# Performance work log

Measured on AMD Instinct MI355X. Metric: run time of the kernel, lower is better.

Reference implementation:

```python
import jax, jax.numpy as jnp
import numpy as np

N_NODES = 100_000
N_EDGES = 1_600_000
D_IN = 128
D_HID = 64   # hard-coded hidden width in Embedder.__init__
D_OUT = 128  # embed_dim
N_GRAPHS = 512


def setup_inputs() -> dict:
    key = jax.random.key(0)
    ks = jax.random.split(key, 10)
    x = jax.random.normal(ks[0], (N_NODES, D_IN), dtype=jnp.float32)
    edge_index = jax.random.randint(ks[1], (2, N_EDGES), 0, N_NODES, dtype=jnp.int64)
    batch_index = jnp.sort(jax.random.randint(ks[2], (N_NODES,), 0, N_GRAPHS, dtype=jnp.int64))
    def glorot(k, fan_in, fan_out):
        s = 1.0 / np.sqrt(fan_in)
        return jax.random.uniform(k, (fan_in, fan_out), jnp.float32, -s, s)
    # layer 1: SAGEConv(D_IN -> D_HID); layer 2: SAGEConv(D_HID -> D_OUT)
    return {
        "x": x,
        "W1_l": glorot(ks[3], D_IN, D_HID),   # applied to mean-aggregated neighbors
        "W1_r": glorot(ks[4], D_IN, D_HID),   # applied to root node
        "b1": jnp.zeros((D_HID,), jnp.float32),
        "W2_l": glorot(ks[5], D_HID, D_OUT),
        "W2_r": glorot(ks[6], D_HID, D_OUT),
        "b2": jnp.zeros((D_OUT,), jnp.float32),
        "edge_index": edge_index,
        "batch_index": batch_index,
    }


def _sage_conv(x, edge_index, W_l, W_r, b):
    # PyG SAGEConv with mean aggregation:
    # out_i = (mean_{j in N(i)} x_j) @ W_l + x_i @ W_r + b
    src, dst = edge_index[0], edge_index[1]
    n = x.shape[0]
    agg = jax.ops.segment_sum(x[src], dst, num_segments=n)          # [N, F]
    deg = jax.ops.segment_sum(jnp.ones((src.shape[0],), x.dtype), dst, num_segments=n)
    mean_nbr = agg / jnp.maximum(deg, 1.0)[:, None]
    return mean_nbr @ W_l + x @ W_r + b


def reference(x, W1_l, W1_r, b1, W2_l, W2_r, b2, edge_index, batch_index):
    h = _sage_conv(x, edge_index, W1_l, W1_r, b1)
    h = jax.nn.relu(h)
    h = _sage_conv(h, edge_index, W2_l, W2_r, b2)
    # F.dropout(p=0.5, training=False) -> identity in eval mode
    # gap: global mean pool per graph
    sums = jax.ops.segment_sum(h, batch_index, num_segments=N_GRAPHS)
    cnts = jax.ops.segment_sum(jnp.ones((h.shape[0],), h.dtype), batch_index, num_segments=N_GRAPHS)
    return sums / jnp.maximum(cnts, 1.0)[:, None]
```

## Files before the change

kernel.cpp:

```cpp
#include <hip/hip_runtime.h>

#define NN   100000
#define NE   1600000
#define DIN  128
#define DH   64
#define DOUT 128
#define NG   512

#define NB   391
#define EPB  6250
#define MSZ  (NB*256)

typedef short short8 __attribute__((ext_vector_type(8)));
typedef float floatx4 __attribute__((ext_vector_type(4)));

__device__ __forceinline__ unsigned short f2bf(float f) {
  unsigned b = __float_as_uint(f);
  b += 0x7FFF + ((b >> 16) & 1);
  return (unsigned short)(b >> 16);
}
__device__ __forceinline__ float bflo(unsigned u) {
  return __uint_as_float(u << 16);
}
__device__ __forceinline__ float bfhi(unsigned u) {
  return __uint_as_float(u & 0xFFFF0000u);
}
__device__ __forceinline__ unsigned pack2(float a, float b) {
  return (unsigned)f2bf(a) | ((unsigned)f2bf(b) << 16);
}

__global__ __launch_bounds__(256) void prep_kernel(
    const int* __restrict__ dst, int* __restrict__ cnt,
    const float* __restrict__ W1l, const float* __restrict__ W1r,
    short* __restrict__ wfrag, const int* __restrict__ batch,
    int* __restrict__ gs) {
  __shared__ int h[NB];
  int b = blockIdx.x;
  if (b < 256) {
    for (int i = threadIdx.x; i < NB; i += 256) h[i] = 0;
    __syncthreads();
    int start = b * EPB, end = start + EPB;
    for (int e = start + threadIdx.x; e < end; e += 256)
      atomicAdd(&h[dst[e] >> 8], 1);
    __syncthreads();
    for (int bb = threadIdx.x; bb < NB; bb += 256)
      cnt[bb * 256 + b] = h[bb];
  } else if (b == 256) {
    for (int i = threadIdx.x; i < DIN * DH; i += 256) {
      int k = i >> 6, n = i & 63;
      int kt = k >> 5, kin = k & 31;
      int lane = ((kin >> 3) << 4) | (n & 15);
      int j8 = kin & 7;
      int jt = n >> 4;
      float wl = W1l[i], wr = W1r[i];
      unsigned bl_ = __float_as_uint(wl);
      unsigned br_ = __float_as_uint(wr);
      short hl = (short)(bl_ >> 16);
      short hr = (short)(br_ >> 16);
      float rl = wl - __uint_as_float(bl_ & 0xFFFF0000u);
      float rr = wr - __uint_as_float(br_ & 0xFFFF0000u);
      short ll = (short)(__float_as_uint(rl) >> 16);
      short lr = (short)(__float_as_uint(rr) >> 16);
      int base0 = (((kt * 2 + 0) * 4 + jt) * 2) * 512 + lane * 8 + j8;
      int base1 = (((kt * 2 + 1) * 4 + jt) * 2) * 512 + lane * 8 + j8;
      wfrag[base0]       = hl;
      wfrag[base0 + 512] = ll;
      wfrag[base1]       = hr;
      wfrag[base1 + 512] = lr;
    }
  } else {
    for (int g = threadIdx.x; g <= NG; g += 256) {
      if (g == NG) { gs[NG] = NN; continue; }
      int lo = 0, hi = NN;
      while (lo < hi) {
        int mid = (lo + hi) >> 1;
        if (batch[mid] < g) lo = mid + 1; else hi = mid;
      }
      gs[g] = lo;
    }
  }
}

__global__ __launch_bounds__(256) void reduce_kernel(
    const int* __restrict__ cnt, int* __restrict__ partials) {
  __shared__ int s[256];
  int i = blockIdx.x * 256 + threadIdx.x;
  s[threadIdx.x] = cnt[i];
  __syncthreads();
  for (int off = 128; off > 0; off >>= 1) {
    if (threadIdx.x < off) s[threadIdx.x] += s[threadIdx.x + off];
    __syncthreads();
  }
  if (threadIdx.x == 0) partials[blockIdx.x] = s[0];
}

__global__ __launch_bounds__(256) void scanpart_kernel(int* __restrict__ partials) {
  __shared__ int s[NB];
  for (int i = threadIdx.x; i < NB; i += 256) s[i] = partials[i];
  __syncthreads();
  if (threadIdx.x == 0) {
    int run = 0;
    for (int i = 0; i < NB; ++i) { int v = s[i]; s[i] = run; run += v; }
  }
  __syncthreads();
  for (int i = threadIdx.x; i < NB; i += 256) partials[i] = s[i];
}

__global__ __launch_bounds__(256) void scanfinal_kernel(
    const int* __restrict__ cnt, const int* __restrict__ partials,
    int* __restrict__ scanned) {
  __shared__ int s[256];
  int t = threadIdx.x;
  int i = blockIdx.x * 256 + t;
  int c = cnt[i];
  s[t] = c;
  __syncthreads();
  for (int off = 1; off < 256; off <<= 1) {
    int v = (t >= off) ? s[t - off] : 0;
    __syncthreads();
    s[t] += v;
    __syncthreads();
  }
  scanned[i] = s[t] - c + partials[blockIdx.x];
}

__global__ __launch_bounds__(1024) void part_kernel(
    const int* __restrict__ src, const int* __restrict__ dst,
    const int* __restrict__ scanned, int* __restrict__ part) {
  __shared__ int cur[NB];
  int b = blockIdx.x;
  for (int i = threadIdx.x; i < NB; i += 1024)
    cur[i] = scanned[i * 256 + b];
  __syncthreads();
  int start = b * EPB, end = start + EPB;
  for (int e = start + threadIdx.x; e < end; e += 1024) {
    int d = dst[e], s = src[e];
    int pos = atomicAdd(&cur[d >> 8], 1);
    part[pos] = ((d & 255) << 17) | s;
  }
}

__global__ __launch_bounds__(256, 5) void proj_kernel(
    const float* __restrict__ x, const short* __restrict__ wfrag,
    const float* __restrict__ b1, unsigned short* __restrict__ xlb,
    unsigned short* __restrict__ xrb) {
  __shared__ short sB[16384];
  int wave = threadIdx.x >> 6;
  int lane = threadIdx.x & 63;
  int m = lane & 15, q = lane >> 4;
  int tile = blockIdx.x * 4 + wave;
  bool act = tile < 6250;
  int tc = act ? tile : 6249;

  int r0 = tc * 16 + m;
  const float4* xa = (const float4*)x + (size_t)r0 * 32 + q * 2;

  floatx4 acc[8];
#pragma unroll
  for (int a = 0; a < 8; ++a) acc[a] = (floatx4){0.f, 0.f, 0.f, 0.f};

  const float4* wf4 = (const float4*)wfrag;
  float4* sB4 = (float4*)sB;

#pragma unroll 1
  for (int stage = 0; stage < 2; ++stage) {
    if (stage) __syncthreads();
    for (int i = threadIdx.x; i < 2048; i += 256)
      sB4[i] = wf4[stage * 2048 + i];
    __syncthreads();

#pragma unroll
    for (int kk = 0; kk < 2; ++kk) {
      int kt = stage * 2 + kk;
      float4 p0 = xa[kt * 8];
      float4 p1 = xa[kt * 8 + 1];
      float af0[8] = {p0.x, p0.y, p0.z, p0.w, p1.x, p1.y, p1.z, p1.w};
      short8 ah, al;
#pragma unroll
      for (int e = 0; e < 8; ++e) {
        unsigned b0 = __float_as_uint(af0[e]);
        ah[e] = (short)(b0 >> 16);
        float lo0 = af0[e] - __uint_as_float(b0 & 0xFFFF0000u);
        al[e] = (short)(__float_as_uint(lo0) >> 16);
      }
#pragma unroll
      for (int mat = 0; mat < 2; ++mat) {
#pragma unroll
        for (int jt = 0; jt < 4; ++jt) {
          int unit = ((kk * 2 + mat) * 4 + jt) * 2;
          short8 bh = *(const short8*)(sB + unit * 512 + lane * 8);
          short8 bl = *(const short8*)(sB + (unit + 1) * 512 + lane * 8);
          floatx4 c = acc[mat * 4 + jt];
          c = __builtin_amdgcn_mfma_f32_16x16x32_bf16(ah, bh, c, 0, 0, 0);
          c = __builtin_amdgcn_mfma_f32_16x16x32_bf16(ah, bl, c, 0, 0, 0);
          c = __builtin_amdgcn_mfma_f32_16x16x32_bf16(al, bh, c, 0, 0, 0);
          acc[mat * 4 + jt] = c;
        }
      }
    }
  }

  if (act) {
#pragma unroll
    for (int jt = 0; jt < 4; ++jt) {
      int j = jt * 16 + m;
      float bj = b1[j];
      floatx4 cl = acc[jt], cr = acc[4 + jt];
#pragma unroll
      for (int r = 0; r < 4; ++r) {
        int n0 = tile * 16 + q * 4 + r;
        xlb[(size_t)n0 * DH + j] = f2bf(cl[r]);
        xrb[(size_t)n0 * DH + j] = f2bf(cr[r] + bj);
      }
    }
  }
}

__global__ __launch_bounds__(256) void bucket_csr_kernel(
    const int* __restrict__ part, const int* __restrict__ scanned,
    int* __restrict__ row_start, int* __restrict__ eidx) {
  int b = blockIdx.x, t = threadIdx.x;
  int ebeg = scanned[b * 256];
  int eend = (b == NB - 1) ? NE : scanned[(b + 1) * 256];
  int nbase = b << 8;
  int nloc = NN - nbase; if (nloc > 256) nloc = 256;
  __shared__ int cntL[256];
  __shared__ int exclL[256];
  cntL[t] = 0;
  __syncthreads();
  for (int e = ebeg + t; e < eend; e += 256)
    atomicAdd(&cntL[part[e] >> 17], 1);
  __syncthreads();
  int c = cntL[t];
  exclL[t] = c;
  __syncthreads();
  for (int off = 1; off < 256; off <<= 1) {
    int v = (t >= off) ? exclL[t - off] : 0;
    __syncthreads();
    exclL[t] += v;
    __syncthreads();
  }
  int excl = exclL[t] - c;
  if (t < nloc) row_start[nbase + t] = ebeg + excl;
  if (b == NB - 1 && t == 0) row_start[NN] = NE;
  cntL[t] = excl;
  __syncthreads();
  for (int e = ebeg + t; e < eend; e += 256) {
    int v = part[e];
    int pos = atomicAdd(&cntL[v >> 17], 1);
    eidx[ebeg + pos] = v & 0x1FFFF;
  }
}

template <bool RELU_ADD>
__global__ __launch_bounds__(256) void gather_kernel(
    const uint4* __restrict__ feat4, const int* __restrict__ row_start,
    const int* __restrict__ eidx, const uint4* __restrict__ xr4,
    uint4* __restrict__ out4) {
  int t = blockIdx.x * 256 + threadIdx.x;
  int node = t >> 3;
  if (node >= NN) return;
  int fl = t & 7;
  int rs = row_start[node], re = row_start[node + 1];
  float a0 = 0.f, a1 = 0.f, a2 = 0.f, a3 = 0.f;
  float a4 = 0.f, a5 = 0.f, a6 = 0.f, a7 = 0.f;
  int k = rs;
  for (; k + 8 <= re; k += 8) {
    uint4 v[8];
#pragma unroll
    for (int u = 0; u < 8; ++u) v[u] = feat4[(size_t)eidx[k + u] * 8 + fl];
#pragma unroll
    for (int u = 0; u < 8; ++u) {
      a0 += bflo(v[u].x); a1 += bfhi(v[u].x);
      a2 += bflo(v[u].y); a3 += bfhi(v[u].y);
      a4 += bflo(v[u].z); a5 += bfhi(v[u].z);
      a6 += bflo(v[u].w); a7 += bfhi(v[u].w);
    }
  }
  for (; k + 2 <= re; k += 2) {
    uint4 v0 = feat4[(size_t)eidx[k] * 8 + fl];
    uint4 v1 = feat4[(size_t)eidx[k + 1] * 8 + fl];
    a0 += bflo(v0.x) + bflo(v1.x); a1 += bfhi(v0.x) + bfhi(v1.x);
    a2 += bflo(v0.y) + bflo(v1.y); a3 += bfhi(v0.y) + bfhi(v1.y);
    a4 += bflo(v0.z) + bflo(v1.z); a5 += bfhi(v0.z) + bfhi(v1.z);
    a6 += bflo(v0.w) + bflo(v1.w); a7 += bfhi(v0.w) + bfhi(v1.w);
  }
  if (k < re) {
    uint4 v = feat4[(size_t)eidx[k] * 8 + fl];
    a0 += bflo(v.x); a1 += bfhi(v.x);
    a2 += bflo(v.y); a3 += bfhi(v.y);
    a4 += bflo(v.z); a5 += bfhi(v.z);
    a6 += bflo(v.w); a7 += bfhi(v.w);
  }
  float inv = 1.0f / fmaxf((float)(re - rs), 1.0f);
  a0 *= inv; a1 *= inv; a2 *= inv; a3 *= inv;
  a4 *= inv; a5 *= inv; a6 *= inv; a7 *= inv;
  if (RELU_ADD) {
    uint4 r = xr4[(size_t)node * 8 + fl];
    a0 = fmaxf(a0 + bflo(r.x), 0.f); a1 = fmaxf(a1 + bfhi(r.x), 0.f);
    a2 = fmaxf(a2 + bflo(r.y), 0.f); a3 = fmaxf(a3 + bfhi(r.y), 0.f);
    a4 = fmaxf(a4 + bflo(r.z), 0.f); a5 = fmaxf(a5 + bfhi(r.z), 0.f);
    a6 = fmaxf(a6 + bflo(r.w), 0.f); a7 = fmaxf(a7 + bfhi(r.w), 0.f);
  }
  uint4 o;
  o.x = pack2(a0, a1);
  o.y = pack2(a2, a3);
  o.z = pack2(a4, a5);
  o.w = pack2(a6, a7);
  out4[(size_t)node * 8 + fl] = o;
}

__global__ __launch_bounds__(256) void pool_final_kernel(
    const unsigned* __restrict__ hb2, const unsigned* __restrict__ mb2,
    const int* __restrict__ gs, const float* __restrict__ W2l,
    const float* __restrict__ W2r, const float* __restrict__ b2,
    float* __restrict__ out) {
  int g = blockIdx.x;
  int start = gs[g], end = gs[g + 1];
  int slot = threadIdx.x >> 5;
  int j2   = threadIdx.x & 31;
  float sh0 = 0.f, sh1 = 0.f, sm0 = 0.f, sm1 = 0.f;
  for (int n = start + slot; n < end; n += 8) {
    unsigned hv = hb2[(size_t)n * 32 + j2];
    unsigned mv = mb2[(size_t)n * 32 + j2];
    sh0 += bflo(hv); sh1 += bfhi(hv);
    sm0 += bflo(mv); sm1 += bfhi(mv);
  }
  __shared__ float redh[8][DH];
  __shared__ float redm[8][DH];
  redh[slot][j2 * 2] = sh0; redh[slot][j2 * 2 + 1] = sh1;
  redm[slot][j2 * 2] = sm0; redm[slot][j2 * 2 + 1] = sm1;
  __syncthreads();
  __shared__ float hsL[DH], msL[DH];
  if (threadIdx.x < DH) {
    float a = 0.f, b = 0.f;
#pragma unroll
    for (int s = 0; s < 8; ++s) { a += redh[s][threadIdx.x]; b += redm[s][threadIdx.x]; }
    hsL[threadIdx.x] = a; msL[threadIdx.x] = b;
  }
  __syncthreads();
  int j = threadIdx.x;
  if (j < DOUT) {
    float n = (float)(end - start);
    float acc = 0.f;
#pragma unroll 8
    for (int k = 0; k < DH; ++k)
      acc += msL[k] * W2l[k * DOUT + j] + hsL[k] * W2r[k * DOUT + j];
    out[g * DOUT + j] = (acc + n * b2[j]) / fmaxf(n, 1.0f);
  }
}

extern "C" void kernel_launch(void* const* d_in, const int* in_sizes, int n_in,
                              void* d_out, int out_size, void* d_ws, size_t ws_size,
                              hipStream_t stream) {
  (void)in_sizes; (void)n_in; (void)out_size; (void)ws_size;
  const float* x   = (const float*)d_in[0];
  const float* W1l = (const float*)d_in[1];
  const float* W1r = (const float*)d_in[2];
  const float* b1  = (const float*)d_in[3];
  const float* W2l = (const float*)d_in[4];
  const float* W2r = (const float*)d_in[5];
  const float* b2  = (const float*)d_in[6];
  const int*   ei  = (const int*)d_in[7];
  const int*   batch = (const int*)d_in[8];
  const int* src = ei;
  const int* dst = ei + NE;
  float* out = (float*)d_out;

  char* ws = (char*)d_ws;
  unsigned short* xlb = (unsigned short*)(ws);
  unsigned short* hb  = (unsigned short*)(ws + 12800000);
  unsigned short* mb  = (unsigned short*)(ws + 25600000);
  unsigned short* xrb = (unsigned short*)(ws + 38400000);
  int*  part      = (int*)(ws + 51200000);
  int*  cnt       = (int*)(ws + 57600000);
  int*  scanned   = (int*)(ws + 58000384);
  int*  eidx      = (int*)(ws + 76800000);
  int*  row_start = (int*)(ws + 83200000);
  int*   gs       = (int*)(ws + 83600128);
  short* wfrag    = (short*)(ws + 83900032);
  int*  partials  = (int*)(ws + 84400128);

  const int gBlocks = (NN * 8 + 255) / 256;

  prep_kernel<<<258, 256, 0, stream>>>(dst, cnt, W1l, W1r, wfrag, batch, gs);
  reduce_kernel<<<NB, 256, 0, stream>>>(cnt, partials);
  scanpart_kernel<<<1, 256, 0, stream>>>(partials);
  scanfinal_kernel<<<NB, 256, 0, stream>>>(cnt, partials, scanned);

  proj_kernel<<<1563, 256, 0, stream>>>(x, wfrag, b1, xlb, xrb);
  part_kernel<<<256, 1024, 0, stream>>>(src, dst, scanned, part);
  bucket_csr_kernel<<<NB, 256, 0, stream>>>(part, scanned, row_start, eidx);

  gather_kernel<true><<<gBlocks, 256, 0, stream>>>(
      (const uint4*)xlb, row_start, eidx, (const uint4*)xrb, (uint4*)hb);

  gather_kernel<false><<<gBlocks, 256, 0, stream>>>(
      (const uint4*)hb, row_start, eidx, nullptr, (uint4*)mb);

  pool_final_kernel<<<NG, 256, 0, stream>>>(
      (const unsigned*)hb, (const unsigned*)mb, gs, W2l, W2r, b2, out);
}
```

Measured before the change: 252.1 us.

## Build CSR with global per-node atomics and fuse scatter into projection kernel

After: 430.4 us. +70.7%, slower.

```diff
diff --git a/kernel.cpp b/kernel.cpp
--- a/kernel.cpp
+++ b/kernel.cpp
@@ -8,8 +8,8 @@
 #define NG   512
 
 #define NB   391
-#define EPB  6250
 #define MSZ  (NB*256)
+#define SCB  1024
 
 typedef short short8 __attribute__((ext_vector_type(8)));
 typedef float floatx4 __attribute__((ext_vector_type(4)));
@@ -30,22 +30,14 @@
 }
 
 __global__ __launch_bounds__(256) void prep_kernel(
-    const int* __restrict__ dst, int* __restrict__ cnt,
+    int* __restrict__ deg,
     const float* __restrict__ W1l, const float* __restrict__ W1r,
     short* __restrict__ wfrag, const int* __restrict__ batch,
     int* __restrict__ gs) {
-  __shared__ int h[NB];
   int b = blockIdx.x;
-  if (b < 256) {
-    for (int i = threadIdx.x; i < NB; i += 256) h[i] = 0;
-    __syncthreads();
-    int start = b * EPB, end = start + EPB;
-    for (int e = start + threadIdx.x; e < end; e += 256)
-      atomicAdd(&h[dst[e] >> 8], 1);
-    __syncthreads();
-    for (int bb = threadIdx.x; bb < NB; bb += 256)
-      cnt[bb * 256 + b] = h[bb];
-  } else if (b == 256) {
+  if (b < NB) {
+    deg[b * 256 + threadIdx.x] = 0;
+  } else if (b == NB) {
     for (int i = threadIdx.x; i < DIN * DH; i += 256) {
       int k = i >> 6, n = i & 63;
       int kt = k >> 5, kin = k & 31;
@@ -81,11 +73,18 @@
   }
 }
 
+__global__ __launch_bounds__(1024) void hist_kernel(
+    const int* __restrict__ dst, int* __restrict__ deg) {
+  int stride = gridDim.x * 1024;
+  for (int e = blockIdx.x * 1024 + threadIdx.x; e < NE; e += stride)
+    atomicAdd(&deg[dst[e]], 1);
+}
+
 __global__ __launch_bounds__(256) void reduce_kernel(
-    const int* __restrict__ cnt, int* __restrict__ partials) {
+    const int* __restrict__ deg, int* __restrict__ partials) {
   __shared__ int s[256];
   int i = blockIdx.x * 256 + threadIdx.x;
-  s[threadIdx.x] = cnt[i];
+  s[threadIdx.x] = deg[i];
   __syncthreads();
   for (int off = 128; off > 0; off >>= 1) {
     if (threadIdx.x < off) s[threadIdx.x] += s[threadIdx.x + off];
@@ -107,12 +106,12 @@
 }
 
 __global__ __launch_bounds__(256) void scanfinal_kernel(
-    const int* __restrict__ cnt, const int* __restrict__ partials,
-    int* __restrict__ scanned) {
+    const int* __restrict__ deg, const int* __restrict__ partials,
+    int* __restrict__ row_start, int* __restrict__ cursor) {
   __shared__ int s[256];
   int t = threadIdx.x;
   int i = blockIdx.x * 256 + t;
-  int c = cnt[i];
+  int c = deg[i];
   s[t] = c;
   __syncthreads();
   for (int off = 1; off < 256; off <<= 1) {
@@ -121,34 +120,30 @@
     s[t] += v;
     __syncthreads();
   }
-  scanned[i] = s[t] - c + partials[blockIdx.x];
-}
-
-__global__ __launch_bounds__(1024) void part_kernel(
+  int val = s[t] - c + partials[blockIdx.x];
+  if (i <= NN) row_start[i] = val;
+  if (i < NN)  cursor[i]    = val;
+}
+
+__global__ __launch_bounds__(256, 5) void proj_scatter_kernel(
     const int* __restrict__ src, const int* __restrict__ dst,
-    const int* __restrict__ scanned, int* __restrict__ part) {
-  __shared__ int cur[NB];
-  int b = blockIdx.x;
-  for (int i = threadIdx.x; i < NB; i += 1024)
-    cur[i] = scanned[i * 256 + b];
-  __syncthreads();
-  int start = b * EPB, end = start + EPB;
-  for (int e = start + threadIdx.x; e < end; e += 1024) {
-    int d = dst[e], s = src[e];
-    int pos = atomicAdd(&cur[d >> 8], 1);
-    part[pos] = ((d & 255) << 17) | s;
-  }
-}
-
-__global__ __launch_bounds__(256, 5) void proj_kernel(
+    int* __restrict__ cursor, int* __restrict__ eidx,
     const float* __restrict__ x, const short* __restrict__ wfrag,
     const float* __restrict__ b1, unsigned short* __restrict__ xlb,
     unsigned short* __restrict__ xrb) {
   __shared__ short sB[16384];
+  if (blockIdx.x < SCB) {
+    for (int e = blockIdx.x * 256 + threadIdx.x; e < NE; e += SCB * 256) {
+      int d = dst[e], s = src[e];
+      int pos = atomicAdd(&cursor[d], 1);
+      eidx[pos] = s;
+    }
+    return;
+  }
   int wave = threadIdx.x >> 6;
   int lane = threadIdx.x & 63;
   int m = lane & 15, q = lane >> 4;
-  int tile = blockIdx.x * 4 + wave;
+  int tile = (blockIdx.x - SCB) * 4 + wave;
   bool act = tile < 6250;
   int tc = act ? tile : 6249;
 
@@ -213,42 +208,6 @@
         xrb[(size_t)n0 * DH + j] = f2bf(cr[r] + bj);
       }
     }
-  }
-}
-
-__global__ __launch_bounds__(256) void bucket_csr_kernel(
-    const int* __restrict__ part, const int* __restrict__ scanned,
-    int* __restrict__ row_start, int* __restrict__ eidx) {
-  int b = blockIdx.x, t = threadIdx.x;
-  int ebeg = scanned[b * 256];
-  int eend = (b == NB - 1) ? NE : scanned[(b + 1) * 256];
-  int nbase = b << 8;
-  int nloc = NN - nbase; if (nloc > 256) nloc = 256;
-  __shared__ int cntL[256];
-  __shared__ int exclL[256];
-  cntL[t] = 0;
-  __syncthreads();
-  for (int e = ebeg + t; e < eend; e += 256)
-    atomicAdd(&cntL[part[e] >> 17], 1);
-  __syncthreads();
-  int c = cntL[t];
-  exclL[t] = c;
-  __syncthreads();
-  for (int off = 1; off < 256; off <<= 1) {
-    int v = (t >= off) ? exclL[t - off] : 0;
-    __syncthreads();
-    exclL[t] += v;
-    __syncthreads();
-  }
-  int excl = exclL[t] - c;
-  if (t < nloc) row_start[nbase + t] = ebeg + excl;
-  if (b == NB - 1 && t == 0) row_start[NN] = NE;
-  cntL[t] = excl;
-  __syncthreads();
-  for (int e = ebeg + t; e < eend; e += 256) {
-    int v = part[e];
-    int pos = atomicAdd(&cntL[v >> 17], 1);
-    eidx[ebeg + pos] = v & 0x1FFFF;
   }
 }
 
@@ -372,9 +331,8 @@
   unsigned short* hb  = (unsigned short*)(ws + 12800000);
   unsigned short* mb  = (unsigned short*)(ws + 25600000);
   unsigned short* xrb = (unsigned short*)(ws + 38400000);
-  int*  part      = (int*)(ws + 51200000);
-  int*  cnt       = (int*)(ws + 57600000);
-  int*  scanned   = (int*)(ws + 58000384);
+  int*  deg       = (int*)(ws + 51200000);
+  int*  cursor    = (int*)(ws + 57600000);
   int*  eidx      = (int*)(ws + 76800000);
   int*  row_start = (int*)(ws + 83200000);
   int*   gs       = (int*)(ws + 83600128);
@@ -383,14 +341,14 @@
 
   const int gBlocks = (NN * 8 + 255) / 256;
 
-  prep_kernel<<<258, 256, 0, stream>>>(dst, cnt, W1l, W1r, wfrag, batch, gs);
-  reduce_kernel<<<NB, 256, 0, stream>>>(cnt, partials);
+  prep_kernel<<<NB + 2, 256, 0, stream>>>(deg, W1l, W1r, wfrag, batch, gs);
+  hist_kernel<<<400, 1024, 0, stream>>>(dst, deg);
+  reduce_kernel<<<NB, 256, 0, stream>>>(deg, partials);
   scanpart_kernel<<<1, 256, 0, stream>>>(partials);
-  scanfinal_kernel<<<NB, 256, 0, stream>>>(cnt, partials, scanned);
-
-  proj_kernel<<<1563, 256, 0, stream>>>(x, wfrag, b1, xlb, xrb);
-  part_kernel<<<256, 1024, 0, stream>>>(src, dst, scanned, part);
-  bucket_csr_kernel<<<NB, 256, 0, stream>>>(part, scanned, row_start, eidx);
+  scanfinal_kernel<<<NB, 256, 0, stream>>>(deg, partials, row_start, cursor);
+
+  proj_scatter_kernel<<<SCB + 1563, 256, 0, stream>>>(
+      src, dst, cursor, eidx, x, wfrag, b1, xlb, xrb);
 
   gather_kernel<true><<<gBlocks, 256, 0, stream>>>(
       (const uint4*)xlb, row_start, eidx, (const uint4*)xrb, (uint4*)hb);
```
